# Kernel tuning notes

Hardware: AMD Instinct MI355X
Metric: run time of the kernel (lower is better)

The kernel has to match this reference:

```python
import jax, jax.numpy as jnp
import numpy as np

INPDIM = 512
RECDIM = 512


def setup_inputs() -> dict:
    key = jax.random.key(0)
    k1, k2, k3, k4 = jax.random.split(key, 4)
    x = jax.random.normal(k1, (64, 1024, INPDIM), dtype=jnp.float32)
    W = jax.random.normal(k2, (INPDIM, RECDIM), dtype=jnp.float32) / np.sqrt(INPDIM)
    # per-unit recurrent weight vector, kept in (-1, 1) for stability
    u = jax.random.uniform(k3, (RECDIM,), dtype=jnp.float32, minval=-1.0, maxval=1.0)
    b = jax.random.normal(k4, (RECDIM,), dtype=jnp.float32) * 0.01
    return {"x": x, "W": W, "u": u, "b": b}


def reference(x, W, u, b):
    # IndRNN: h_t = relu(x_t @ W + u * h_{t-1} + b), h_0 = ones(recdim)
    B, T, _ = x.shape
    # Batch the input projection as one big GEMM (time-independent part).
    xp = jnp.einsum('bti,ir->btr', x, W) + b  # [B, T, R]
    h0 = jnp.ones((B, W.shape[1]), dtype=x.dtype)

    def step(h, xp_t):
        h = jax.nn.relu(xp_t + u * h)
        return h, h

    _, hs = jax.lax.scan(step, h0, jnp.swapaxes(xp, 0, 1))  # hs: [T, B, R]
    return jnp.swapaxes(hs, 0, 1)  # [B, T, R]
```

## Files before the change

kernel.cpp:

```cpp
#include <hip/hip_runtime.h>
#include <hip/hip_fp16.h>
#include <hip/hip_bf16.h>
#include <stdint.h>

#define TILE 128
#define BK 32
#define LDST 40

typedef __attribute__((ext_vector_type(8))) short short8;
typedef __attribute__((ext_vector_type(8))) unsigned short ushort8;
typedef __attribute__((ext_vector_type(4))) float f32x4;

typedef const __attribute__((address_space(1))) void* gptr_t;
typedef __attribute__((address_space(3))) void* lptr_t;

static __device__ __forceinline__ unsigned short f2bf(float f) {
    union { float f; uint32_t u; } v; v.f = f;
    uint32_t u = v.u;
    u += 0x7fffu + ((u >> 16) & 1u);
    return (unsigned short)(u >> 16);
}

static __device__ __forceinline__ unsigned int pk_bf16(float a, float b) {
    __hip_bfloat162 h = __float22bfloat162_rn(float2{a, b});
    union { __hip_bfloat162 h; unsigned int u; } c; c.h = h;
    return c.u;
}

__global__ __launch_bounds__(256)
void wt_kernel(const float* __restrict__ W, unsigned short* __restrict__ Wt)
{
    __shared__ float s[32][33];
    const int tx = threadIdx.x;
    const int ty = threadIdx.y;
    const int kBase = blockIdx.x * 32;
    const int nBase = blockIdx.y * 32;
    #pragma unroll
    for (int j = 0; j < 4; ++j)
        s[ty + 8 * j][tx] = W[(size_t)(kBase + ty + 8 * j) * 512 + nBase + tx];
    __syncthreads();
    #pragma unroll
    for (int j = 0; j < 4; ++j)
        Wt[(size_t)(nBase + ty + 8 * j) * 512 + kBase + tx] = f2bf(s[tx][ty + 8 * j]);
}

__global__ __launch_bounds__(256)
void xb_kernel(const float* __restrict__ X, unsigned short* __restrict__ Xb)
{
    size_t i = ((size_t)blockIdx.x * 256 + threadIdx.x) * 16;
    const size_t stride = (size_t)2048 * 256 * 16;
    #pragma unroll
    for (int it = 0; it < 4; ++it, i += stride) {
        float4 v0 = *(const float4*)(X + i);
        float4 v1 = *(const float4*)(X + i + 4);
        float4 v2 = *(const float4*)(X + i + 8);
        float4 v3 = *(const float4*)(X + i + 12);
        union { ushort8 s8; unsigned int u[4]; } a, b;
        a.u[0] = pk_bf16(v0.x, v0.y); a.u[1] = pk_bf16(v0.z, v0.w);
        a.u[2] = pk_bf16(v1.x, v1.y); a.u[3] = pk_bf16(v1.z, v1.w);
        b.u[0] = pk_bf16(v2.x, v2.y); b.u[1] = pk_bf16(v2.z, v2.w);
        b.u[2] = pk_bf16(v3.x, v3.y); b.u[3] = pk_bf16(v3.z, v3.w);
        *(ushort8*)(Xb + i)     = a.s8;
        *(ushort8*)(Xb + i + 8) = b.s8;
    }
}

__global__ __launch_bounds__(256, 2)
void gemm_xb_kernel(const unsigned short* __restrict__ Xb, const unsigned short* __restrict__ Wt,
                    const float* __restrict__ bias, __half* __restrict__ xpT)
{
    __shared__ unsigned short As[TILE * BK];
    __shared__ unsigned short Bs[TILE * BK];

    const int tid = threadIdx.x;

    const int lin = blockIdx.x;
    const int xcd = lin & 7;
    const int idx = lin >> 3;
    const int rowBase = (xcd * 64 + (idx >> 2)) * TILE;
    const int colBase = (idx & 3) * TILE;

    const int wave  = tid >> 6;
    const int lane  = tid & 63;
    const int m16   = lane & 15;
    const int quad  = lane >> 4;
    const int waveM = wave & 1;
    const int waveN = wave >> 1;

    f32x4 acc[4][4] = {};

    const int c0 = wave * 2 * 64 + lane;
    const int m0 = c0 >> 2, j0 = c0 & 3;
    const int c1 = (wave * 2 + 1) * 64 + lane;
    const int m1 = c1 >> 2, j1 = c1 & 3;

    const unsigned short* aS0 = Xb + (size_t)(rowBase + m0) * 512 + j0 * 8;
    const unsigned short* aS1 = Xb + (size_t)(rowBase + m1) * 512 + j1 * 8;
    const unsigned short* bS0 = Wt + (size_t)(colBase + m0) * 512 + j0 * 8;
    const unsigned short* bS1 = Wt + (size_t)(colBase + m1) * 512 + j1 * 8;

    for (int kt = 0; kt < 512; kt += BK) {
        __builtin_amdgcn_global_load_lds((gptr_t)(aS0 + kt),
            (lptr_t)((char*)As + (wave * 2) * 64 * 16), 16, 0, 0);
        __builtin_amdgcn_global_load_lds((gptr_t)(aS1 + kt),
            (lptr_t)((char*)As + (wave * 2 + 1) * 64 * 16), 16, 0, 0);
        __builtin_amdgcn_global_load_lds((gptr_t)(bS0 + kt),
            (lptr_t)((char*)Bs + (wave * 2) * 64 * 16), 16, 0, 0);
        __builtin_amdgcn_global_load_lds((gptr_t)(bS1 + kt),
            (lptr_t)((char*)Bs + (wave * 2 + 1) * 64 * 16), 16, 0, 0);
        __syncthreads();

        short8 a_frag[4], b_frag[4];
        #pragma unroll
        for (int mi = 0; mi < 4; ++mi)
            a_frag[mi] = *(const short8*)&As[(waveM * 64 + mi * 16 + m16) * BK + quad * 8];
        #pragma unroll
        for (int ni = 0; ni < 4; ++ni)
            b_frag[ni] = *(const short8*)&Bs[(waveN * 64 + ni * 16 + m16) * BK + quad * 8];

        #pragma unroll
        for (int mi = 0; mi < 4; ++mi)
            #pragma unroll
            for (int ni = 0; ni < 4; ++ni)
                acc[mi][ni] = __builtin_amdgcn_mfma_f32_16x16x32_bf16(
                    b_frag[ni], a_frag[mi], acc[mi][ni], 0, 0, 0);
        __syncthreads();
    }

    const int bb = rowBase >> 10;
    #pragma unroll
    for (int ni = 0; ni < 4; ++ni) {
        int r0 = colBase + waveN * 64 + ni * 16 + quad * 4;
        float4 b4 = *(const float4*)&bias[r0];
        #pragma unroll
        for (int mi = 0; mi < 4; ++mi) {
            int tt = (rowBase + waveM * 64 + mi * 16 + m16) & 1023;
            #pragma unroll
            for (int r = 0; r < 4; ++r) {
                float v = acc[mi][ni][r] + ((const float*)&b4)[r];
                xpT[((size_t)bb * 512 + r0 + r) * 1024 + tt] = __float2half_rn(v);
            }
        }
    }
}

__global__ __launch_bounds__(256, 2)
void gemm_f32_kernel(const float* __restrict__ X, const unsigned short* __restrict__ Wt,
                     const float* __restrict__ bias, float* __restrict__ out32)
{
    __shared__ unsigned short As[TILE * LDST];
    __shared__ unsigned short Bs[TILE * LDST];

    const int tid = threadIdx.x;
    const int lin = blockIdx.x;
    const int xcd = lin & 7;
    const int idx = lin >> 3;
    const int rowBase = (xcd * 64 + (idx >> 2)) * TILE;
    const int colBase = (idx & 3) * TILE;

    const int wave  = tid >> 6;
    const int lane  = tid & 63;
    const int m16   = lane & 15;
    const int quad  = lane >> 4;
    const int waveM = wave & 1;
    const int waveN = wave >> 1;

    f32x4 acc[4][4] = {};

    const int srow = tid >> 2;
    const int sc4  = tid & 3;

    for (int kt = 0; kt < 512; kt += BK) {
        #pragma unroll
        for (int p = 0; p < 2; ++p) {
            int r = p * 64 + srow;
            const float* src = X + (size_t)(rowBase + r) * 512 + kt + sc4 * 8;
            float4 v0 = *(const float4*)(src);
            float4 v1 = *(const float4*)(src + 4);
            union { ushort8 s8; unsigned int u[4]; } us;
            us.u[0] = pk_bf16(v0.x, v0.y); us.u[1] = pk_bf16(v0.z, v0.w);
            us.u[2] = pk_bf16(v1.x, v1.y); us.u[3] = pk_bf16(v1.z, v1.w);
            *(ushort8*)(&As[r * LDST + sc4 * 8]) = us.s8;
        }
        #pragma unroll
        for (int p = 0; p < 2; ++p) {
            int n = p * 64 + srow;
            ushort8 v = *(const ushort8*)(Wt + (size_t)(colBase + n) * 512 + kt + sc4 * 8);
            *(ushort8*)(&Bs[n * LDST + sc4 * 8]) = v;
        }
        __syncthreads();

        short8 a_frag[4], b_frag[4];
        #pragma unroll
        for (int mi = 0; mi < 4; ++mi)
            a_frag[mi] = *(const short8*)&As[(waveM * 64 + mi * 16 + m16) * LDST + quad * 8];
        #pragma unroll
        for (int ni = 0; ni < 4; ++ni)
            b_frag[ni] = *(const short8*)&Bs[(waveN * 64 + ni * 16 + m16) * LDST + quad * 8];

        #pragma unroll
        for (int mi = 0; mi < 4; ++mi)
            #pragma unroll
            for (int ni = 0; ni < 4; ++ni)
                acc[mi][ni] = __builtin_amdgcn_mfma_f32_16x16x32_bf16(
                    a_frag[mi], b_frag[ni], acc[mi][ni], 0, 0, 0);
        __syncthreads();
    }

    #pragma unroll
    for (int ni = 0; ni < 4; ++ni) {
        int col = colBase + waveN * 64 + ni * 16 + m16;
        float bv = bias[col];
        #pragma unroll
        for (int mi = 0; mi < 4; ++mi) {
            int row0 = rowBase + waveM * 64 + mi * 16 + quad * 4;
            #pragma unroll
            for (int r = 0; r < 4; ++r) {
                float v = acc[mi][ni][r] + bv;
                out32[(size_t)(row0 + r) * 512 + col] = v;
            }
        }
    }
}

#define SUNR 128

__global__ __launch_bounds__(64)
void scan_t_kernel(const __half* __restrict__ xpT, float* __restrict__ out,
                   const float* __restrict__ u)
{
    const int gid = blockIdx.x * 64 + threadIdx.x;
    const int b = gid >> 9;
    const int r = gid & 511;
    const float ur = u[r];
    const unsigned short* p = (const unsigned short*)xpT + ((size_t)b * 512 + r) * 1024;
    float* po = out + (size_t)b * 1024 * 512 + r;

    float h = 1.0f;
    ushort8 cur[SUNR / 8], nxt[SUNR / 8];
    #pragma unroll
    for (int j = 0; j < SUNR / 8; ++j) cur[j] = *(const ushort8*)(p + j * 8);

    for (int t0 = 0; t0 < 1024; t0 += SUNR) {
        const bool more = (t0 + SUNR) < 1024;
        if (more) {
            #pragma unroll
            for (int j = 0; j < SUNR / 8; ++j)
                nxt[j] = *(const ushort8*)(p + t0 + SUNR + j * 8);
        }
        #pragma unroll
        for (int j = 0; j < SUNR / 8; ++j) {
            #pragma unroll
            for (int e = 0; e < 8; ++e) {
                float xv = __half2float(__ushort_as_half(cur[j][e]));
                h = fmaxf(fmaf(ur, h, xv), 0.0f);
                __builtin_nontemporal_store(h, po + (size_t)(t0 + j * 8 + e) * 512);
            }
        }
        #pragma unroll
        for (int j = 0; j < SUNR / 8; ++j) cur[j] = nxt[j];
    }
}

#define UNR 32
__global__ __launch_bounds__(64)
void scan_f32_kernel(float* __restrict__ out, const float* __restrict__ u)
{
    const int gid = blockIdx.x * 64 + threadIdx.x;
    const int b = gid >> 9;
    const int r = gid & 511;
    const float ur = u[r];
    float* p = out + (size_t)b * 1024 * 512 + r;

    float h = 1.0f;
    float cur[UNR], nxt[UNR];
    #pragma unroll
    for (int j = 0; j < UNR; ++j) cur[j] = p[(size_t)j * 512];

    for (int t0 = 0; t0 < 1024; t0 += UNR) {
        const bool more = (t0 + UNR) < 1024;
        const float* pn = p + (size_t)(t0 + UNR) * 512;
        if (more) {
            #pragma unroll
            for (int j = 0; j < UNR; ++j) nxt[j] = pn[(size_t)j * 512];
        }
        #pragma unroll
        for (int j = 0; j < UNR; ++j) {
            h = fmaxf(fmaf(ur, h, cur[j]), 0.0f);
            p[(size_t)(t0 + j) * 512] = h;
        }
        #pragma unroll
        for (int j = 0; j < UNR; ++j) cur[j] = nxt[j];
    }
}

extern "C" void kernel_launch(void* const* d_in, const int* in_sizes, int n_in,
                              void* d_out, int out_size, void* d_ws, size_t ws_size,
                              hipStream_t stream) {
    const float* x = (const float*)d_in[0];
    const float* W = (const float*)d_in[1];
    const float* u = (const float*)d_in[2];
    const float* b = (const float*)d_in[3];
    float* out = (float*)d_out;

    const size_t WT_BYTES = (size_t)512 * 512 * 2;
    const size_t XP_BYTES = (size_t)64 * 1024 * 512 * 2;
    unsigned short* Wt = (unsigned short*)d_ws;
    __half* xp16 = (__half*)((char*)d_ws + WT_BYTES);
    const bool f16path = ws_size >= WT_BYTES + XP_BYTES;

    dim3 tgrid(16, 16), tblk(32, 8);
    wt_kernel<<<tgrid, tblk, 0, stream>>>(W, Wt);

    if (f16path) {
        unsigned short* Xb = (unsigned short*)out;
        xb_kernel<<<2048, 256, 0, stream>>>(x, Xb);
        gemm_xb_kernel<<<2048, 256, 0, stream>>>(Xb, Wt, b, xp16);
        scan_t_kernel<<<512, 64, 0, stream>>>(xp16, out, u);
    } else {
        gemm_f32_kernel<<<2048, 256, 0, stream>>>(x, Wt, b, out);
        scan_f32_kernel<<<512, 64, 0, stream>>>(out, u);
    }
}
```

Measured before the change: 291.7 us.

## Triple-buffer GEMM LDS tiles with async global_load_lds prefetch two stages ahead

Turns the single-buffered K loop of the input-projection GEMM into a three-stage LDS ring. Loads for tile t+2 are issued before computing tile t, with explicit vmcnt waits and a single barrier per iteration. This is meant to hide global-to-LDS load latency behind MFMA work and to remove one barrier per iteration. LDS use triples to 48KB per block, which may limit occupancy, and correctness depends on the vmcnt counts and barrier placement being right.

Measured after the change: 293.6 us. About the same (+0.6%).

```diff
diff --git a/kernel.cpp b/kernel.cpp
--- a/kernel.cpp
+++ b/kernel.cpp
@@ -69,8 +69,8 @@
 void gemm_xb_kernel(const unsigned short* __restrict__ Xb, const unsigned short* __restrict__ Wt,
                     const float* __restrict__ bias, __half* __restrict__ xpT)
 {
-    __shared__ unsigned short As[TILE * BK];
-    __shared__ unsigned short Bs[TILE * BK];
+    __shared__ unsigned short As[3][TILE * BK];
+    __shared__ unsigned short Bs[3][TILE * BK];
 
     const int tid = threadIdx.x;
 
@@ -93,39 +93,56 @@
     const int m0 = c0 >> 2, j0 = c0 & 3;
     const int c1 = (wave * 2 + 1) * 64 + lane;
     const int m1 = c1 >> 2, j1 = c1 & 3;
+    const int cb0 = (wave * 2) * 64 * 16;
+    const int cb1 = (wave * 2 + 1) * 64 * 16;
 
     const unsigned short* aS0 = Xb + (size_t)(rowBase + m0) * 512 + j0 * 8;
     const unsigned short* aS1 = Xb + (size_t)(rowBase + m1) * 512 + j1 * 8;
     const unsigned short* bS0 = Wt + (size_t)(colBase + m0) * 512 + j0 * 8;
     const unsigned short* bS1 = Wt + (size_t)(colBase + m1) * 512 + j1 * 8;
 
-    for (int kt = 0; kt < 512; kt += BK) {
-        __builtin_amdgcn_global_load_lds((gptr_t)(aS0 + kt),
-            (lptr_t)((char*)As + (wave * 2) * 64 * 16), 16, 0, 0);
-        __builtin_amdgcn_global_load_lds((gptr_t)(aS1 + kt),
-            (lptr_t)((char*)As + (wave * 2 + 1) * 64 * 16), 16, 0, 0);
-        __builtin_amdgcn_global_load_lds((gptr_t)(bS0 + kt),
-            (lptr_t)((char*)Bs + (wave * 2) * 64 * 16), 16, 0, 0);
-        __builtin_amdgcn_global_load_lds((gptr_t)(bS1 + kt),
-            (lptr_t)((char*)Bs + (wave * 2 + 1) * 64 * 16), 16, 0, 0);
-        __syncthreads();
-
-        short8 a_frag[4], b_frag[4];
-        #pragma unroll
-        for (int mi = 0; mi < 4; ++mi)
-            a_frag[mi] = *(const short8*)&As[(waveM * 64 + mi * 16 + m16) * BK + quad * 8];
-        #pragma unroll
-        for (int ni = 0; ni < 4; ++ni)
-            b_frag[ni] = *(const short8*)&Bs[(waveN * 64 + ni * 16 + m16) * BK + quad * 8];
-
-        #pragma unroll
-        for (int mi = 0; mi < 4; ++mi)
-            #pragma unroll
-            for (int ni = 0; ni < 4; ++ni)
-                acc[mi][ni] = __builtin_amdgcn_mfma_f32_16x16x32_bf16(
-                    b_frag[ni], a_frag[mi], acc[mi][ni], 0, 0, 0);
-        __syncthreads();
-    }
+#define STAGE(bufi, ko)                                                                          \
+    __builtin_amdgcn_global_load_lds((gptr_t)(aS0 + (ko)), (lptr_t)((char*)As[bufi] + cb0), 16, 0, 0); \
+    __builtin_amdgcn_global_load_lds((gptr_t)(aS1 + (ko)), (lptr_t)((char*)As[bufi] + cb1), 16, 0, 0); \
+    __builtin_amdgcn_global_load_lds((gptr_t)(bS0 + (ko)), (lptr_t)((char*)Bs[bufi] + cb0), 16, 0, 0); \
+    __builtin_amdgcn_global_load_lds((gptr_t)(bS1 + (ko)), (lptr_t)((char*)Bs[bufi] + cb1), 16, 0, 0)
+
+#define COMPUTE(bufi)                                                                            \
+    {                                                                                            \
+        short8 a_frag[4], b_frag[4];                                                             \
+        _Pragma("unroll")                                                                        \
+        for (int mi = 0; mi < 4; ++mi)                                                           \
+            a_frag[mi] = *(const short8*)&As[bufi][(waveM * 64 + mi * 16 + m16) * BK + quad * 8];\
+        _Pragma("unroll")                                                                        \
+        for (int ni = 0; ni < 4; ++ni)                                                           \
+            b_frag[ni] = *(const short8*)&Bs[bufi][(waveN * 64 + ni * 16 + m16) * BK + quad * 8];\
+        _Pragma("unroll")                                                                        \
+        for (int mi = 0; mi < 4; ++mi)                                                           \
+            _Pragma("unroll")                                                                    \
+            for (int ni = 0; ni < 4; ++ni)                \
+                acc[mi][ni] = __builtin_amdgcn_mfma_f32_16x16x32_bf16(                           \
+                    b_frag[ni], a_frag[mi], acc[mi][ni], 0, 0, 0);                               \
+    }
+
+    STAGE(0, 0);
+    STAGE(1, BK);
+    asm volatile("s_waitcnt vmcnt(4)" ::: "memory");
+    __builtin_amdgcn_s_barrier();
+
+    for (int t = 0; t < 14; ++t) {
+        const int kt = t * BK;
+        STAGE((t + 2) % 3, kt + 2 * BK);
+        COMPUTE(t % 3);
+        asm volatile("s_waitcnt vmcnt(4)" ::: "memory");
+        __builtin_amdgcn_s_barrier();
+    }
+    COMPUTE(2);
+    asm volatile("s_waitcnt vmcnt(0)" ::: "memory");
+    __builtin_amdgcn_s_barrier();
+    COMPUTE(0);
+
+#undef STAGE
+#undef COMPUTE
 
     const int bb = rowBase >> 10;
     #pragma unroll
```
